# Optimization experiments

Measured on AMD Instinct MI355X. Metric: run time of the kernel, lower is better.

The kernel has to match this reference:

```python
import jax, jax.numpy as jnp
import numpy as np

N_QUBITS = 14
N_LAYERS = 3
DIM = 1 << N_QUBITS


def _butterfly(state, q, g00, g01, g10, g11):
    # Apply 2x2 gate on qubit q (bit mask 1<<q). Gate entries may be scalars or [B] arrays.
    B, dim = state.shape
    low = 1 << q
    high = dim >> (q + 1)
    s = state.reshape(B, high, 2, low)
    a0, a1 = s[:, :, 0, :], s[:, :, 1, :]
    def bb(g):
        g = jnp.asarray(g)
        return g.reshape(-1, 1, 1) if g.ndim == 1 else g
    b0 = bb(g00) * a0 + bb(g01) * a1
    b1 = bb(g10) * a0 + bb(g11) * a1
    return jnp.stack([b0, b1], axis=2).reshape(B, dim)


def _rx(state, q, angle):
    c = jnp.cos(angle / 2)
    s = jnp.sin(angle / 2)
    return _butterfly(state, q, c + 0j, -1j * s, -1j * s, c + 0j)


def _ry(state, q, angle):
    c = jnp.cos(angle / 2)
    s = jnp.sin(angle / 2)
    return _butterfly(state, q, c + 0j, -s + 0j, s + 0j, c + 0j)


def _rz(state, q, angle):
    # bit=1 amplitudes get exp(+i a/2), bit=0 get exp(-i a/2)
    p = jnp.exp(1j * angle / 2)
    B, dim = state.shape
    low = 1 << q
    high = dim >> (q + 1)
    s = state.reshape(B, high, 2, low)
    s0 = s[:, :, 0, :] * jnp.conj(p)
    s1 = s[:, :, 1, :] * p
    return jnp.stack([s0, s1], axis=2).reshape(B, dim)


def _pcnot(state, control, target, angle):
    # Where control bit is 1: new[i] = cos*a[i] + 1j*sin*a[i ^ target_mask]; else unchanged.
    B, dim = state.shape
    low = 1 << target
    high = dim >> (target + 1)
    swapped = state.reshape(B, high, 2, low)[:, :, ::-1, :].reshape(B, dim)
    full = jnp.cos(angle) * state + 1j * jnp.sin(angle) * swapped
    idx = jnp.arange(dim)
    cmask = ((idx >> control) & 1).astype(bool)
    return jnp.where(cmask[None, :], full, state)


def setup_inputs() -> dict:
    key = jax.random.key(0)
    ks = jax.random.split(key, 10)
    return {
        "x": jax.random.normal(ks[0], (1024, 64), jnp.float32),
        "encoding_params": jax.random.normal(ks[1], (64, N_QUBITS), jnp.float32),
        "rot_params": jax.random.normal(ks[2], (N_LAYERS, N_QUBITS, 3), jnp.float32),
        "ent_params": jax.random.normal(ks[3], (N_LAYERS, N_QUBITS - 1), jnp.float32),
        "w1": jax.random.normal(ks[4], (DIM, 256), jnp.float32),
        "b1": jax.random.normal(ks[5], (256,), jnp.float32),
        "w2": jax.random.normal(ks[6], (256, 128), jnp.float32),
        "b2": jax.random.normal(ks[7], (128,), jnp.float32),
        "w3": jax.random.normal(ks[8], (128, 64), jnp.float32),
        "b3": jax.random.normal(ks[9], (64,), jnp.float32),
    }


def reference(x, encoding_params, rot_params, ent_params, w1, b1, w2, b2, w3, b3):
    B = x.shape[0]
    n = N_QUBITS
    # |0...0> initial state
    state = jnp.zeros((B, DIM), jnp.complex64).at[:, 0].set(1.0)
    # data encoding: RY(angle_q) per qubit, batch-dependent angles
    enc_angles = x @ encoding_params  # [B, n_qubits]
    for q in range(n):
        state = _ry(state, q, enc_angles[:, q])
    # parameterized layers
    for l in range(N_LAYERS):
        for q in range(n):
            state = _rx(state, q, rot_params[l, q, 0])
            state = _ry(state, q, rot_params[l, q, 1])
            state = _rz(state, q, rot_params[l, q, 2])
        # circular entanglement: last gate uses angle 0 (identity), as in original
        for i in range(n):
            control, target = i, (i + 1) % n
            angle = ent_params[l, i] if i < n - 1 else jnp.float32(0.0)
            state = _pcnot(state, control, target, angle)
    # measurement: probabilities |amp|^2
    feats = jnp.abs(state) ** 2  # [B, DIM] float32
    h = jax.nn.relu(feats @ w1 + b1)
    h = jax.nn.relu(h @ w2 + b2)
    return h @ w3 + b3
```

## Files before the change

kernel.cpp:

```cpp
#include <hip/hip_runtime.h>
#include <hip/hip_bf16.h>
#include <cstdint>
#include <cstddef>

#define NQ      14
#define SDIM    16384
#define NGATES  39
#define NBATCH  1024
#define KSPLIT  16
#define GENT    42

typedef short bf16x8 __attribute__((ext_vector_type(8)));
typedef float f32x4  __attribute__((ext_vector_type(4)));
typedef __fp16 half2v __attribute__((ext_vector_type(2)));

__device__ __forceinline__ float2 cmul(float2 a, float2 b) {
    return make_float2(fmaf(a.x, b.x, -a.y * b.y), fmaf(a.x, b.y, a.y * b.x));
}
__device__ __forceinline__ void cfma(float2 &o, float2 a, float2 b) {
    o.x = fmaf(a.x, b.x, fmaf(-a.y, b.y, o.x));
    o.y = fmaf(a.x, b.y, fmaf( a.y, b.x, o.y));
}

__device__ __forceinline__ unsigned cmul16(unsigned c, unsigned a) {
    unsigned t, o;
    asm("v_pk_mul_f16 %0, %2, %3 op_sel:[0,0] op_sel_hi:[0,1]\n\t"
        "v_pk_fma_f16 %1, %2, %3, %0 op_sel:[1,1,0] op_sel_hi:[1,0,1] neg_lo:[1,0,0]"
        : "=&v"(t), "=v"(o) : "s"(c), "v"(a));
    return o;
}
__device__ __forceinline__ void cfma16(unsigned &o, unsigned c, unsigned a) {
    unsigned t;
    asm("v_pk_fma_f16 %0, %2, %3, %1 op_sel:[0,0,0] op_sel_hi:[0,1,1]\n\t"
        "v_pk_fma_f16 %1, %2, %3, %0 op_sel:[1,1,0] op_sel_hi:[1,0,1] neg_lo:[1,0,0]"
        : "=&v"(t), "+v"(o) : "s"(c), "v"(a));
}

__device__ void mm2(const float2 A[2][2], const float2 B[2][2], float2 C[2][2]) {
    #pragma unroll
    for (int i = 0; i < 2; ++i)
        #pragma unroll
        for (int j = 0; j < 2; ++j) {
            float2 t = cmul(A[i][0], B[0][j]);
            cfma(t, A[i][1], B[1][j]);
            C[i][j] = t;
        }
}

__device__ void build_u(const float* __restrict__ rp, const float* __restrict__ enc,
                        int l, int q, float2 U[2][2]) {
    const float* p = rp + (l * NQ + q) * 3;
    float ha = 0.5f * p[0], hb = 0.5f * p[1], hg = 0.5f * p[2];
    float cx = cosf(ha), sx = sinf(ha);
    float cy = cosf(hb), sy = sinf(hb);
    float cz = cosf(hg), sz = sinf(hg);
    float2 RX[2][2] = { { make_float2(cx, 0.f), make_float2(0.f, -sx) },
                        { make_float2(0.f, -sx), make_float2(cx, 0.f) } };
    float2 RY[2][2] = { { make_float2(cy, 0.f), make_float2(-sy, 0.f) },
                        { make_float2(sy, 0.f), make_float2(cy, 0.f) } };
    float2 W[2][2];
    mm2(RY, RX, W);
    float2 zl = make_float2(cz, -sz), zh = make_float2(cz, sz);
    float2 V[2][2];
    V[0][0] = cmul(zl, W[0][0]); V[0][1] = cmul(zl, W[0][1]);
    V[1][0] = cmul(zh, W[1][0]); V[1][1] = cmul(zh, W[1][1]);
    if (l == 0) {
        float he = 0.5f * enc[q];
        float ce = cosf(he), se = sinf(he);
        float2 RE[2][2] = { { make_float2(ce, 0.f), make_float2(-se, 0.f) },
                            { make_float2(se, 0.f), make_float2(ce, 0.f) } };
        mm2(V, RE, U);
    } else {
        U[0][0] = V[0][0]; U[0][1] = V[0][1];
        U[1][0] = V[1][0]; U[1][1] = V[1][1];
    }
}

__device__ __forceinline__ unsigned pkh(float2 f) {
    half2v h = __builtin_amdgcn_cvt_pkrtz(f.x, f.y);
    return *(unsigned*)&h;
}

__global__ __launch_bounds__(256) void prep_wtr_kernel(
    const float* __restrict__ x,
    const float* __restrict__ ep,
    const float* __restrict__ rp,
    const float* __restrict__ ent,
    const float* __restrict__ w1,
    unsigned* __restrict__ gtab,
    __hip_bfloat16* __restrict__ w1t)
{
    __shared__ float tile[64][65];
    __shared__ float angles[NQ];
    const int b = blockIdx.x, t = threadIdx.x;
    const int kb = (b >> 2) * 64, nb = (b & 3) * 64;

    #pragma unroll
    for (int i = 0; i < 16; ++i) {
        int idx = t + i * 256; int r = idx >> 6, c = idx & 63;
        tile[r][c] = w1[(size_t)(kb + r) * 256 + nb + c];
    }
    if (t < NQ) {
        float a = 0.f;
        const float* xr = x + (size_t)b * 64;
        #pragma unroll 8
        for (int k = 0; k < 64; ++k) a = fmaf(xr[k], ep[k * NQ + t], a);
        angles[t] = a;
    }
    __syncthreads();

    #pragma unroll
    for (int i = 0; i < 16; ++i) {
        int idx = t + i * 256; int n = idx >> 6, k = idx & 63;
        w1t[(size_t)(nb + n) * SDIM + kb + k] = __float2bfloat16(tile[k][n]);
    }

    unsigned* G0 = gtab + (size_t)b * (GENT * 8);
    if (t < NGATES) {
        int l = t / 13, jj = t - l * 13;
        float2 Ut[2][2];
        build_u(rp, angles, l, jj + 1, Ut);
        float th = ent[l * 13 + jj];
        float ct = cosf(th), s = sinf(th);
        unsigned* G = G0 + t * 8;
        G[0] = pkh(Ut[0][0]); G[1] = pkh(Ut[0][1]); G[2] = pkh(Ut[1][0]); G[3] = pkh(Ut[1][1]);
        G[4] = pkh(make_float2(fmaf(ct, Ut[0][0].x, -s * Ut[1][0].y), fmaf(ct, Ut[0][0].y, s * Ut[1][0].x)));
        G[5] = pkh(make_float2(fmaf(ct, Ut[0][1].x, -s * Ut[1][1].y), fmaf(ct, Ut[0][1].y, s * Ut[1][1].x)));
        G[6] = pkh(make_float2(fmaf(ct, Ut[1][0].x, -s * Ut[0][0].y), fmaf(ct, Ut[1][0].y, s * Ut[0][0].x)));
        G[7] = pkh(make_float2(fmaf(ct, Ut[1][1].x, -s * Ut[0][1].y), fmaf(ct, Ut[1][1].y, s * Ut[0][1].x)));
    } else if (t < GENT) {
        int l = t - NGATES;
        float2 U[2][2];
        build_u(rp, angles, l, 0, U);
        unsigned* D = G0 + t * 8;
        D[0] = pkh(U[0][0]); D[1] = pkh(U[0][1]); D[2] = pkh(U[1][0]); D[3] = pkh(U[1][1]);
    }
}

template<int CP>
__device__ __forceinline__ void gate_sparse8(unsigned v[16], const unsigned* __restrict__ G) {
    {
        unsigned c00 = G[0], c01 = G[1], c10 = G[2], c11 = G[3];
        #pragma unroll
        for (int rr = 0; rr < 4; ++rr) {
            const int base = ((rr >> CP) << (CP + 2)) | (rr & ((1 << CP) - 1));
            const int m0 = base, m2 = base | (2 << CP);
            unsigned a0 = v[m0], a2 = v[m2];
            unsigned o0 = cmul16(c00, a0); cfma16(o0, c01, a2);
            unsigned o2 = cmul16(c10, a0); cfma16(o2, c11, a2);
            v[m0] = o0; v[m2] = o2;
        }
    }
    {
        unsigned c00 = G[4], c01 = G[5], c10 = G[6], c11 = G[7];
        #pragma unroll
        for (int rr = 0; rr < 4; ++rr) {
            const int base = ((rr >> CP) << (CP + 2)) | (rr & ((1 << CP) - 1));
            const int m1 = base | (1 << CP), m3 = base | (3 << CP);
            unsigned a1 = v[m1], a3 = v[m3];
            unsigned o1 = cmul16(c00, a1); cfma16(o1, c01, a3);
            unsigned o3 = cmul16(c10, a1); cfma16(o3, c11, a3);
            v[m1] = o1; v[m3] = o3;
        }
    }
}

template<int P> __device__ __forceinline__ int pass_i0(int tid) {
    if constexpr (P == 0) return ((tid & 15) << 5) | (tid & 16) | ((tid & 32) << 4) | ((tid & 0x3C0) << 4);
    if constexpr (P == 1) return (tid & 7) | (((tid >> 4) & 1) << 7) | (((tid >> 3) & 1) << 8)
                               | (((tid >> 5) & 1) << 9) | ((tid >> 6) << 10);
    if constexpr (P == 2) return (tid & 63) | ((tid >> 6) << 10);
    if constexpr (P == 3) return (tid & 31) | (((tid >> 6) & 15) << 5) | (((tid >> 5) & 1) << 13);
    if constexpr (P == 4) return (tid & 31) | (((tid >> 6) & 15) << 5) | (((tid >> 5) & 1) << 9);
    return 0;
}
template<int P> __device__ __forceinline__ constexpr int pass_cj(int j) {
    if constexpr (P == 0) return j * 4;
    if constexpr (P == 1) return (((j << 3) | (j >> 2))) * 4;
    if constexpr (P == 2) return (((j << 6) | (j << 1))) * 4;
    if constexpr (P == 3) return (((j << 9) | ((j & 1) << 4))) * 4;
    if constexpr (P == 4) return (j << 10) * 4;
    return 0;
}

template<int P, bool INIT, bool U0F, bool EMIT>
__device__ __forceinline__ void passT(char* __restrict__ smemc,
                                      const unsigned* __restrict__ gb,
                                      const unsigned* __restrict__ u0,
                                      __hip_bfloat16* __restrict__ fr, int tid) {
    const int i0   = pass_i0<P>(tid);
    const int base = (i0 ^ ((i0 >> 5) & 31)) * 4;

    unsigned v[16];
    if (INIT) {
        #pragma unroll
        for (int j = 0; j < 16; ++j) v[j] = 0u;
        if (tid == 0) v[0] = 0x3C00u;
    } else {
        #pragma unroll
        for (int j = 0; j < 16; ++j)
            v[j] = *(const unsigned*)(smemc + (base ^ pass_cj<P>(j)));
    }

    if (U0F) {
        unsigned u00 = u0[0], u01 = u0[1], u10 = u0[2], u11 = u0[3];
        #pragma unroll
        for (int k = 0; k < 8; ++k) {
            unsigned e = v[2 * k], o = v[2 * k + 1];
            unsigned ne = cmul16(u00, e); cfma16(ne, u01, o);
            unsigned no = cmul16(u10, e); cfma16(no, u11, o);
            v[2 * k] = ne; v[2 * k + 1] = no;
        }
    }

    if (P < 4) {
        gate_sparse8<0>(v, gb);
        gate_sparse8<1>(v, gb + 8);
        gate_sparse8<2>(v, gb + 16);
    } else {
        gate_sparse8<2>(v, gb);
    }

    if (EMIT) {
        #pragma unroll
        for (int j = 0; j < 16; ++j) {
            half2v h = *(half2v*)&v[j];
            float re = (float)h.x, im = (float)h.y;
            fr[i0 + (j << 10)] = __float2bfloat16(fmaf(re, re, im * im));
        }
    } else {
        #pragma unroll
        for (int j = 0; j < 16; ++j)
            *(unsigned*)(smemc + (base ^ pass_cj<P>(j))) = v[j];
    }
}

__global__ __launch_bounds__(1024) __attribute__((amdgpu_waves_per_eu(8, 8)))
void sim_kernel(
    const unsigned* __restrict__ gtab,
    __hip_bfloat16* __restrict__ feats)
{
    __shared__ unsigned int st[SDIM];

    char* smemc = (char*)st;
    const int tid = threadIdx.x;
    const int b   = blockIdx.x;

    const unsigned* gt = gtab + (size_t)b * (GENT * 8);
    __hip_bfloat16* fr = feats + (size_t)b * SDIM;

    {
        const unsigned* gl = gt;
        passT<0, true,  true,  false>(smemc, gl,          gt + 39 * 8, nullptr, tid); __syncthreads();
        passT<1, false, false, false>(smemc, gl + 3 * 8,  nullptr,     nullptr, tid); __syncthreads();
        passT<2, false, false, false>(smemc, gl + 6 * 8,  nullptr,     nullptr, tid); __syncthreads();
        passT<3, false, false, false>(smemc, gl + 9 * 8,  nullptr,     nullptr, tid); __syncthreads();
        passT<4, false, false, false>(smemc, gl + 12 * 8, nullptr,     nullptr, tid); __syncthreads();
    }
    {
        const unsigned* gl = gt + 13 * 8;
        passT<0, false, true,  false>(smemc, gl,          gt + 40 * 8, nullptr, tid); __syncthreads();
        passT<1, false, false, false>(smemc, gl + 3 * 8,  nullptr,     nullptr, tid); __syncthreads();
        passT<2, false, false, false>(smemc, gl + 6 * 8,  nullptr,     nullptr, tid); __syncthreads();
        passT<3, false, false, false>(smemc, gl + 9 * 8,  nullptr,     nullptr, tid); __syncthreads();
        passT<4, false, false, false>(smemc, gl + 12 * 8, nullptr,     nullptr, tid); __syncthreads();
    }
    {
        const unsigned* gl = gt + 26 * 8;
        passT<0, false, true,  false>(smemc, gl,          gt + 41 * 8, nullptr, tid); __syncthreads();
        passT<1, false, false, false>(smemc, gl + 3 * 8,  nullptr,     nullptr, tid); __syncthreads();
        passT<2, false, false, false>(smemc, gl + 6 * 8,  nullptr,     nullptr, tid); __syncthreads();
        passT<3, false, false, false>(smemc, gl + 9 * 8,  nullptr,     nullptr, tid); __syncthreads();
        passT<4, false, false, true >(smemc, gl + 12 * 8, nullptr,     fr,      tid);
    }
}

__global__ __launch_bounds__(256) void gemm1_mfma(
    const __hip_bfloat16* __restrict__ A,
    const __hip_bfloat16* __restrict__ B,
    float* __restrict__ part)
{
    __shared__ char As[8192];
    __shared__ char Bs[8192];
    const int tid  = threadIdx.x;
    const int lane = tid & 63;
    const int wave = tid >> 6;
    const int wm = wave & 1, wn = wave >> 1;
    const int bm = blockIdx.x, bn = blockIdx.y, ks = blockIdx.z;
    const int k0 = ks * 1024;

    const int c0 = tid, c1 = tid + 256;
    const int r0s = c0 >> 2, kb0 = (c0 & 3) ^ ((r0s >> 1) & 3);
    const int r1s = c1 >> 2, kb1 = (c1 & 3) ^ ((r1s >> 1) & 3);
    const __hip_bfloat16* A0 = A + (size_t)(bm * 128 + r0s) * SDIM + k0 + kb0 * 8;
    const __hip_bfloat16* A1 = A + (size_t)(bm * 128 + r1s) * SDIM + k0 + kb1 * 8;
    const __hip_bfloat16* B0 = B + (size_t)(bn * 128 + r0s) * SDIM + k0 + kb0 * 8;
    const __hip_bfloat16* B1 = B + (size_t)(bn * 128 + r1s) * SDIM + k0 + kb1 * 8;

    const int kbx  = lane >> 4;
    const int arow = wm * 64 + (lane & 15);
    const int brow = wn * 64 + (lane & 15);
    const int abase = arow * 64 + ((kbx ^ ((arow >> 1) & 3)) << 4);
    const int bbase = brow * 64 + ((kbx ^ ((brow >> 1) & 3)) << 4);

    f32x4 acc[4][4];
    #pragma unroll
    for (int i = 0; i < 4; ++i)
        #pragma unroll
        for (int j = 0; j < 4; ++j)
            acc[i][j] = (f32x4){0.f, 0.f, 0.f, 0.f};

    uint4 ra0 = *(const uint4*)A0;
    uint4 ra1 = *(const uint4*)A1;
    uint4 rb0 = *(const uint4*)B0;
    uint4 rb1 = *(const uint4*)B1;

    for (int kt = 0; kt < 32; ++kt) {
        *(uint4*)(As + c0 * 16) = ra0;
        *(uint4*)(As + c1 * 16) = ra1;
        *(uint4*)(Bs + c0 * 16) = rb0;
        *(uint4*)(Bs + c1 * 16) = rb1;
        __syncthreads();
        if (kt < 31) {
            const int d = (kt + 1) * 32;
            ra0 = *(const uint4*)(A0 + d);
            ra1 = *(const uint4*)(A1 + d);
            rb0 = *(const uint4*)(B0 + d);
            rb1 = *(const uint4*)(B1 + d);
        }
        bf16x8 a[4], b[4];
        #pragma unroll
        for (int mi = 0; mi < 4; ++mi) a[mi] = *(const bf16x8*)(As + abase + mi * 1024);
        #pragma unroll
        for (int ni = 0; ni < 4; ++ni) b[ni] = *(const bf16x8*)(Bs + bbase + ni * 1024);
        #pragma unroll
        for (int mi = 0; mi < 4; ++mi)
            #pragma unroll
            for (int ni = 0; ni < 4; ++ni)
                acc[mi][ni] = __builtin_amdgcn_mfma_f32_16x16x32_bf16(a[mi], b[ni], acc[mi][ni], 0, 0, 0);
        __syncthreads();
    }

    float* P = part + ((size_t)ks * NBATCH + bm * 128 + wm * 64) * 256 + bn * 128 + wn * 64;
    const int mrow = (lane >> 4) * 4;
    const int ncol = lane & 15;
    #pragma unroll
    for (int mi = 0; mi < 4; ++mi)
        #pragma unroll
        for (int ni = 0; ni < 4; ++ni) {
            #pragma unroll
            for (int r = 0; r < 4; ++r)
                P[(size_t)(mi * 16 + mrow + r) * 256 + ni * 16 + ncol] = acc[mi][ni][r];
        }
}

__global__ __launch_bounds__(256) void tail_kernel(
    const float* __restrict__ part,
    const float* __restrict__ b1,
    const float* __restrict__ w2,
    const float* __restrict__ b2,
    const float* __restrict__ w3,
    const float* __restrict__ b3,
    float* __restrict__ out)
{
    __shared__ float h1[256];
    __shared__ float h2[128];
    const int b = blockIdx.x, t = threadIdx.x;

    float s = b1[t];
    #pragma unroll
    for (int sp = 0; sp < KSPLIT; ++sp)
        s += part[((size_t)sp * NBATCH + b) * 256 + t];
    h1[t] = fmaxf(s, 0.f);
    __syncthreads();

    if (t < 128) {
        float acc = b2[t];
        #pragma unroll 4
        for (int k = 0; k < 256; ++k) acc = fmaf(h1[k], w2[k * 128 + t], acc);
        h2[t] = fmaxf(acc, 0.f);
    }
    __syncthreads();

    if (t < 64) {
        float acc = b3[t];
        #pragma unroll 4
        for (int k = 0; k < 128; ++k) acc = fmaf(h2[k], w3[k * 64 + t], acc);
        out[(size_t)b * 64 + t] = acc;
    }
}

extern "C" void kernel_launch(void* const* d_in, const int* in_sizes, int n_in,
                              void* d_out, int out_size, void* d_ws, size_t ws_size,
                              hipStream_t stream) {
    const float* x   = (const float*)d_in[0];
    const float* ep  = (const float*)d_in[1];
    const float* rp  = (const float*)d_in[2];
    const float* ent = (const float*)d_in[3];
    const float* w1  = (const float*)d_in[4];
    const float* b1  = (const float*)d_in[5];
    const float* w2  = (const float*)d_in[6];
    const float* b2  = (const float*)d_in[7];
    const float* w3  = (const float*)d_in[8];
    const float* b3  = (const float*)d_in[9];
    float* out = (float*)d_out;

    __hip_bfloat16* feats = (__hip_bfloat16*)d_ws;
    __hip_bfloat16* w1t   = feats + (size_t)NBATCH * SDIM;
    float*          part  = (float*)(w1t + (size_t)256 * SDIM);
    unsigned*       gtab  = (unsigned*)(part + (size_t)KSPLIT * NBATCH * 256);

    prep_wtr_kernel<<<NBATCH, 256, 0, stream>>>(x, ep, rp, ent, w1, gtab, w1t);
    sim_kernel<<<NBATCH, 1024, 0, stream>>>(gtab, feats);
    gemm1_mfma<<<dim3(8, 2, KSPLIT), 256, 0, stream>>>(feats, w1t, part);
    tail_kernel<<<NBATCH, 256, 0, stream>>>(part, b1, w2, b2, w3, b3, out);
}
```

Measured before the change: 159.7 us.

## Fuse W1 transpose and bf16 conversion into GEMM operand loading

Removes the separate w1 transpose/bf16 pass from the prep kernel. The GEMM now reads fp32 W1 directly with strided loads, converts to bf16 in registers, and writes the transposed layout into shared memory. The GEMM block grows to 512 threads, each wave covering 32 rows instead of 64, and the prep kernel shrinks to 64 threads. This saves a 16 MB read plus an 8 MB write of workspace traffic. The cost is uncoalesced scalar fp32 loads of W1 inside the GEMM, which also reads twice as many bytes for B.

```diff
diff --git a/kernel.cpp b/kernel.cpp
--- a/kernel.cpp
+++ b/kernel.cpp
@@ -81,25 +81,16 @@
     return *(unsigned*)&h;
 }
 
-__global__ __launch_bounds__(256) void prep_wtr_kernel(
+__global__ __launch_bounds__(64) void prep_kernel(
     const float* __restrict__ x,
     const float* __restrict__ ep,
     const float* __restrict__ rp,
     const float* __restrict__ ent,
-    const float* __restrict__ w1,
-    unsigned* __restrict__ gtab,
-    __hip_bfloat16* __restrict__ w1t)
+    unsigned* __restrict__ gtab)
 {
-    __shared__ float tile[64][65];
     __shared__ float angles[NQ];
     const int b = blockIdx.x, t = threadIdx.x;
-    const int kb = (b >> 2) * 64, nb = (b & 3) * 64;
-
-    #pragma unroll
-    for (int i = 0; i < 16; ++i) {
-        int idx = t + i * 256; int r = idx >> 6, c = idx & 63;
-        tile[r][c] = w1[(size_t)(kb + r) * 256 + nb + c];
-    }
+
     if (t < NQ) {
         float a = 0.f;
         const float* xr = x + (size_t)b * 64;
@@ -108,12 +99,6 @@
         angles[t] = a;
     }
     __syncthreads();
-
-    #pragma unroll
-    for (int i = 0; i < 16; ++i) {
-        int idx = t + i * 256; int n = idx >> 6, k = idx & 63;
-        w1t[(size_t)(nb + n) * SDIM + kb + k] = __float2bfloat16(tile[k][n]);
-    }
 
     unsigned* G0 = gtab + (size_t)b * (GENT * 8);
     if (t < NGATES) {
@@ -275,9 +260,9 @@
     }
 }
 
-__global__ __launch_bounds__(256) void gemm1_mfma(
+__global__ __launch_bounds__(512) void gemm1_mfma(
     const __hip_bfloat16* __restrict__ A,
-    const __hip_bfloat16* __restrict__ B,
+    const float* __restrict__ W1,
     float* __restrict__ part)
 {
     __shared__ char As[8192];
@@ -285,67 +270,72 @@
     const int tid  = threadIdx.x;
     const int lane = tid & 63;
     const int wave = tid >> 6;
-    const int wm = wave & 1, wn = wave >> 1;
+    const int wm = wave >> 1, wn = wave & 1;
     const int bm = blockIdx.x, bn = blockIdx.y, ks = blockIdx.z;
     const int k0 = ks * 1024;
 
-    const int c0 = tid, c1 = tid + 256;
-    const int r0s = c0 >> 2, kb0 = (c0 & 3) ^ ((r0s >> 1) & 3);
-    const int r1s = c1 >> 2, kb1 = (c1 & 3) ^ ((r1s >> 1) & 3);
-    const __hip_bfloat16* A0 = A + (size_t)(bm * 128 + r0s) * SDIM + k0 + kb0 * 8;
-    const __hip_bfloat16* A1 = A + (size_t)(bm * 128 + r1s) * SDIM + k0 + kb1 * 8;
-    const __hip_bfloat16* B0 = B + (size_t)(bn * 128 + r0s) * SDIM + k0 + kb0 * 8;
-    const __hip_bfloat16* B1 = B + (size_t)(bn * 128 + r1s) * SDIM + k0 + kb1 * 8;
+    const int ra_ = tid >> 2, kba = (tid & 3) ^ ((ra_ >> 1) & 3);
+    const __hip_bfloat16* Ap = A + (size_t)(bm * 128 + ra_) * SDIM + k0 + kba * 8;
+    const int nb_ = tid >> 2, kbb = (tid & 3) ^ ((nb_ >> 1) & 3);
+    const float* Bp = W1 + (size_t)(k0 + kbb * 8) * 256 + bn * 128 + nb_;
 
     const int kbx  = lane >> 4;
-    const int arow = wm * 64 + (lane & 15);
+    const int arow = wm * 32 + (lane & 15);
     const int brow = wn * 64 + (lane & 15);
     const int abase = arow * 64 + ((kbx ^ ((arow >> 1) & 3)) << 4);
     const int bbase = brow * 64 + ((kbx ^ ((brow >> 1) & 3)) << 4);
 
-    f32x4 acc[4][4];
+    f32x4 acc[2][4];
     #pragma unroll
-    for (int i = 0; i < 4; ++i)
+    for (int i = 0; i < 2; ++i)
         #pragma unroll
         for (int j = 0; j < 4; ++j)
             acc[i][j] = (f32x4){0.f, 0.f, 0.f, 0.f};
 
-    uint4 ra0 = *(const uint4*)A0;
-    uint4 ra1 = *(const uint4*)A1;
-    uint4 rb0 = *(const uint4*)B0;
-    uint4 rb1 = *(const uint4*)B1;
+    uint4 ra = *(const uint4*)Ap;
+    float rb[8];
+    #pragma unroll
+    for (int j = 0; j < 8; ++j) rb[j] = Bp[(size_t)j * 256];
 
     for (int kt = 0; kt < 32; ++kt) {
-        *(uint4*)(As + c0 * 16) = ra0;
-        *(uint4*)(As + c1 * 16) = ra1;
-        *(uint4*)(Bs + c0 * 16) = rb0;
-        *(uint4*)(Bs + c1 * 16) = rb1;
+        uint4 bw;
+        {
+            unsigned u[4];
+            #pragma unroll
+            for (int i = 0; i < 4; ++i) {
+                __hip_bfloat16 h0 = __float2bfloat16(rb[2 * i]);
+                __hip_bfloat16 h1 = __float2bfloat16(rb[2 * i + 1]);
+                u[i] = (unsigned)*(unsigned short*)&h0 | ((unsigned)*(unsigned short*)&h1 << 16);
+            }
+            bw = make_uint4(u[0], u[1], u[2], u[3]);
+        }
+        *(uint4*)(As + tid * 16) = ra;
+        *(uint4*)(Bs + tid * 16) = bw;
         __syncthreads();
         if (kt < 31) {
             const int d = (kt + 1) * 32;
-            ra0 = *(const uint4*)(A0 + d);
-            ra1 = *(const uint4*)(A1 + d);
-            rb0 = *(const uint4*)(B0 + d);
-            rb1 = *(const uint4*)(B1 + d);
-        }
-        bf16x8 a[4], b[4];
-        #pragma unroll
-        for (int mi = 0; mi < 4; ++mi) a[mi] = *(const bf16x8*)(As + abase + mi * 1024);
+            ra = *(const uint4*)(Ap + d);
+            #pragma unroll
+            for (int j = 0; j < 8; ++j) rb[j] = Bp[((size_t)d + j) * 256];
+        }
+        bf16x8 a[2], b[4];
+        #pragma unroll
+        for (int mi = 0; mi < 2; ++mi) a[mi] = *(const bf16x8*)(As + abase + mi * 1024);
         #pragma unroll
         for (int ni = 0; ni < 4; ++ni) b[ni] = *(const bf16x8*)(Bs + bbase + ni * 1024);
         #pragma unroll
-        for (int mi = 0; mi < 4; ++mi)
+        for (int mi = 0; mi < 2; ++mi)
             #pragma unroll
             for (int ni = 0; ni < 4; ++ni)
                 acc[mi][ni] = __builtin_amdgcn_mfma_f32_16x16x32_bf16(a[mi], b[ni], acc[mi][ni], 0, 0, 0);
         __syncthreads();
     }
 
-    float* P = part + ((size_t)ks * NBATCH + bm * 128 + wm * 64) * 256 + bn * 128 + wn * 64;
+    float* P = part + ((size_t)ks * NBATCH + bm * 128 + wm * 32) * 256 + bn * 128 + wn * 64;
     const int mrow = (lane >> 4) * 4;
     const int ncol = lane & 15;
     #pragma unroll
-    for (int mi = 0; mi < 4; ++mi)
+    for (int mi = 0; mi < 2; ++mi)
         #pragma unroll
         for (int ni = 0; ni < 4; ++ni) {
             #pragma unroll
@@ -406,12 +396,11 @@
     float* out = (float*)d_out;
 
     __hip_bfloat16* feats = (__hip_bfloat16*)d_ws;
-    __hip_bfloat16* w1t   = feats + (size_t)NBATCH * SDIM;
-    float*          part  = (float*)(w1t + (size_t)256 * SDIM);
+    float*          part  = (float*)(feats + (size_t)NBATCH * SDIM);
     unsigned*       gtab  = (unsigned*)(part + (size_t)KSPLIT * NBATCH * 256);
 
-    prep_wtr_kernel<<<NBATCH, 256, 0, stream>>>(x, ep, rp, ent, w1, gtab, w1t);
+    prep_kernel<<<NBATCH, 64, 0, stream>>>(x, ep, rp, ent, gtab);
     sim_kernel<<<NBATCH, 1024, 0, stream>>>(gtab, feats);
-    gemm1_mfma<<<dim3(8, 2, KSPLIT), 256, 0, stream>>>(feats, w1t, part);
+    gemm1_mfma<<<dim3(8, 2, KSPLIT), 512, 0, stream>>>(feats, w1, part);
     tail_kernel<<<NBATCH, 256, 0, stream>>>(part, b1, w2, b2, w3, b3, out);
 }
```

Result: slower. 171.3 us (+7.2%).
